# Kernel optimization log

Measured on AMD Instinct MI355X. Metric: run time of the kernel, lower is better.

The kernel has to match this reference:

```python
import jax, jax.numpy as jnp
import numpy as np

N, E, IN_FT, OUT_FT = 20000, 4096, 128, 128


def setup_inputs() -> dict:
    key = jax.random.key(0)
    kx, kh, kw = jax.random.split(key, 3)
    X = jax.random.normal(kx, (N, IN_FT), dtype=jnp.float32)
    H = jax.random.randint(kh, (N, E), 0, 2, dtype=jnp.int32)
    weight = jax.random.normal(kw, (IN_FT, OUT_FT), dtype=jnp.float32) * (1.0 / np.sqrt(IN_FT))
    bias = jnp.zeros((OUT_FT,), dtype=jnp.float32)
    return {"X": X, "H": H, "weight": weight, "bias": bias}


def reference(X, H, weight, bias):
    # Dv^{-1/2} H De^{-1} H^T Dv^{-1/2} X W + b, with diag matrices fused as
    # row/column scalings (same math as the torch.diag @ chain, no NxN temporaries).
    Hf = H.astype(jnp.float32)
    v_deg = jnp.sum(Hf, axis=1)            # [N]
    e_deg = jnp.sum(Hf, axis=0)            # [E]
    v_deg = jnp.where(v_deg > 0, v_deg, 1.0)
    e_deg = jnp.where(e_deg > 0, e_deg, 1.0)
    dv_inv_sqrt = 1.0 / jnp.sqrt(v_deg)    # diag(Dv^-1/2)
    de_inv = 1.0 / e_deg                   # diag(De^-1)
    Y = dv_inv_sqrt[:, None] * X
    T = Hf.T @ Y                           # H^T (...)        [E, in]
    T = de_inv[:, None] * T                # De^-1 (...)
    Z = Hf @ T                             # H (...)          [N, in]
    Z = dv_inv_sqrt[:, None] * Z           # Dv^-1/2 (...)
    out = Z @ weight + bias                # [N, out]
    return out
```

## Files before the change

### kernel.cpp

```cpp
#include <hip/hip_runtime.h>

#define NV 20000
#define NE 4096
#define FT 128
#define NW_E 128
#define NW_V 625
#define PT_STRIDE 632
#define NKC2 157
#define K_TOT 20096

typedef __attribute__((ext_vector_type(8))) short short8v;
typedef __attribute__((ext_vector_type(4))) float float4v;

__device__ __forceinline__ unsigned short f2bf(float f) {
    unsigned u = __float_as_uint(f);
    u += 0x7FFFu + ((u >> 16) & 1u);
    return (unsigned short)(u >> 16);
}
__device__ __forceinline__ int lds_off(int r, int c) {
    return r * 256 + ((c ^ (r & 15)) << 4);
}
__device__ __forceinline__ uint4 lut_entry(int t) {
    uint4 e;
    e.x = ((t & 1) ? 0x3F80u : 0u) | ((t & 2) ? 0x3F800000u : 0u);
    e.y = ((t & 4) ? 0x3F80u : 0u) | ((t & 8) ? 0x3F800000u : 0u);
    e.z = ((t & 16) ? 0x3F80u : 0u) | ((t & 32) ? 0x3F800000u : 0u);
    e.w = ((t & 64) ? 0x3F80u : 0u) | ((t & 128) ? 0x3F800000u : 0u);
    return e;
}
__device__ __forceinline__ void cp16(void* l, const void* g) {
    __builtin_amdgcn_global_load_lds((__attribute__((address_space(1))) void*)g,
                                     (__attribute__((address_space(3))) void*)l, 16, 0, 0);
}

__global__ __launch_bounds__(256) void k_pack(const int* __restrict__ H,
                                              unsigned* __restrict__ packed,
                                              float* __restrict__ dv,
                                              int* __restrict__ de_cnt) {
    __shared__ int cl[4];
    int t = threadIdx.x, wave = t >> 6, lane = t & 63;
    if (blockIdx.x < 16) de_cnt[blockIdx.x * 256 + t] = 0;
    int row = blockIdx.x * 2 + (wave >> 1);
    int half = wave & 1;
    const uint4* base = reinterpret_cast<const uint4*>(H) + (size_t)row * 1024 + half * 512 + lane * 8;
    unsigned m = 0;
#pragma unroll
    for (int i = 0; i < 8; ++i) {
        uint4 v = base[i];
        m |= (v.x ? 1u : 0u) << (i * 4 + 0);
        m |= (v.y ? 1u : 0u) << (i * 4 + 1);
        m |= (v.z ? 1u : 0u) << (i * 4 + 2);
        m |= (v.w ? 1u : 0u) << (i * 4 + 3);
    }
    packed[(size_t)row * NW_E + half * 64 + lane] = m;
    int c = __popc(m);
    for (int o = 32; o > 0; o >>= 1) c += __shfl_down(c, o, 64);
    if (lane == 0) cl[wave] = c;
    __syncthreads();
    if (t < 2) {
        int d = cl[t * 2] + cl[t * 2 + 1];
        dv[blockIdx.x * 2 + t] = d > 0 ? 1.0f / sqrtf((float)d) : 1.0f;
    }
}

__global__ __launch_bounds__(256) void k_btrans(const unsigned* __restrict__ packed,
                                                unsigned* __restrict__ packedT,
                                                int* __restrict__ de_cnt) {
    int lane = threadIdx.x & 63;
    int w = threadIdx.x >> 6;
    int ew = blockIdx.y * 4 + w;
    int n = blockIdx.x * 64 + lane;
    unsigned x = (n < NV) ? packed[(size_t)n * NW_E + ew] : 0u;
    unsigned y;
    y = __shfl_xor(x, 16, 64);
    x = (lane & 16) ? ((x & 0xFFFF0000u) | ((y >> 16) & 0x0000FFFFu))
                    : ((x & 0x0000FFFFu) | ((y << 16) & 0xFFFF0000u));
    y = __shfl_xor(x, 8, 64);
    x = (lane & 8)  ? ((x & 0xFF00FF00u) | ((y >> 8) & 0x00FF00FFu))
                    : ((x & 0x00FF00FFu) | ((y << 8) & 0xFF00FF00u));
    y = __shfl_xor(x, 4, 64);
    x = (lane & 4)  ? ((x & 0xF0F0F0F0u) | ((y >> 4) & 0x0F0F0F0Fu))
                    : ((x & 0x0F0F0F0Fu) | ((y << 4) & 0xF0F0F0F0u));
    y = __shfl_xor(x, 2, 64);
    x = (lane & 2)  ? ((x & 0xCCCCCCCCu) | ((y >> 2) & 0x33333333u))
                    : ((x & 0x33333333u) | ((y << 2) & 0xCCCCCCCCu));
    y = __shfl_xor(x, 1, 64);
    x = (lane & 1)  ? ((x & 0xAAAAAAAAu) | ((y >> 1) & 0x55555555u))
                    : ((x & 0x55555555u) | ((y << 1) & 0xAAAAAAAAu));
    int nw = blockIdx.x * 2 + (lane >> 5);
    int e = ew * 32 + (lane & 31);
    if (nw <= 625) packedT[(size_t)e * PT_STRIDE + nw] = x;
    int cnt = __popc(x);
    cnt += __shfl_down(cnt, 32, 64);
    if (lane < 32) atomicAdd(de_cnt + e, cnt);
}

__global__ __launch_bounds__(256) void k_mid(const float* __restrict__ X,
                                             const float* __restrict__ dv,
                                             unsigned short* __restrict__ At) {
    int t = threadIdx.x;
    int f = t & 127;
    int item = blockIdx.x * 2 + (t >> 7);
    int nbase = item * 8;
    unsigned short h[8];
#pragma unroll
    for (int i = 0; i < 8; ++i) {
        int n = nbase + i;
        float v = (n < NV) ? X[(size_t)n * FT + f] * dv[n] : 0.0f;
        h[i] = f2bf(v);
    }
    uint4 u;
    u.x = (unsigned)h[0] | ((unsigned)h[1] << 16);
    u.y = (unsigned)h[2] | ((unsigned)h[3] << 16);
    u.z = (unsigned)h[4] | ((unsigned)h[5] << 16);
    u.w = (unsigned)h[6] | ((unsigned)h[7] << 16);
    int kc2 = nbase >> 7;
    int c = (nbase >> 3) & 15;
    *reinterpret_cast<uint4*>(At + (size_t)kc2 * 16384 + f * 128 + ((c ^ (f & 15)) << 3)) = u;
}

__global__ __launch_bounds__(256, 2) void k_mm1(const unsigned short* __restrict__ At,
                                                const unsigned* __restrict__ packedT,
                                                float* __restrict__ P, int chunkK) {
    __shared__ __align__(16) unsigned char sA[32768];
    __shared__ __align__(16) unsigned char sB[32768];
    __shared__ __align__(16) uint4 slut[256];
    int t = threadIdx.x;
    slut[t] = lut_entry(t);

    int et = blockIdx.x & 31, kp = blockIdx.x >> 5;
    int e0 = et * 128;
    int kbeg = kp * chunkK;
    int kend = kbeg + chunkK; if (kend > K_TOT) kend = K_TOT;
    int iters = (kend - kbeg) >> 7; if (iters < 0) iters = 0;

    float4v acc[4][4];
#pragma unroll
    for (int i = 0; i < 4; ++i)
#pragma unroll
        for (int j = 0; j < 4; ++j)
#pragma unroll
            for (int r = 0; r < 4; ++r) acc[i][j][r] = 0.0f;

    int wave = t >> 6, lane = t & 63;
    int wm0 = (wave & 1) * 64, wc0 = (wave >> 1) * 64;
    int r0 = lane & 15, q = lane >> 4;

    int rB = t & 127, half = t >> 7, cb = half << 3;
    const uint4* brow4 = reinterpret_cast<const uint4*>(
        packedT + (size_t)(e0 + rB) * PT_STRIDE + (kbeg >> 5));
    uint4 bw;
    if (iters > 0) bw = brow4[0];
    __syncthreads();

    const char* gA = reinterpret_cast<const char*>(At) + (size_t)(kbeg >> 7) * 32768 + wave * 8192 + lane * 16;
    char* lA = reinterpret_cast<char*>(sA) + wave * 8192;

    for (int it = 0; it < iters; ++it) {
        const char* g = gA + (size_t)it * 32768;
#pragma unroll
        for (int j = 0; j < 8; ++j) cp16(lA + j * 1024, g + j * 1024);
        {
            uint4 nxt = brow4[it + 1];
            unsigned wd0 = half ? bw.z : bw.x;
            unsigned wd1 = half ? bw.w : bw.y;
#pragma unroll
            for (int c = 0; c < 4; ++c)
                *reinterpret_cast<uint4*>(sB + lds_off(rB, cb + c)) = slut[(wd0 >> (c * 8)) & 0xFF];
#pragma unroll
            for (int c = 0; c < 4; ++c)
                *reinterpret_cast<uint4*>(sB + lds_off(rB, cb + 4 + c)) = slut[(wd1 >> (c * 8)) & 0xFF];
            bw = nxt;
        }
        __syncthreads();
#pragma unroll
        for (int ks = 0; ks < 4; ++ks) {
            short8v a[4], bb[4];
#pragma unroll
            for (int mi = 0; mi < 4; ++mi)
                a[mi] = *reinterpret_cast<const short8v*>(sA + lds_off(wm0 + mi * 16 + r0, ks * 4 + q));
#pragma unroll
            for (int ci = 0; ci < 4; ++ci)
                bb[ci] = *reinterpret_cast<const short8v*>(sB + lds_off(wc0 + ci * 16 + r0, ks * 4 + q));
#pragma unroll
            for (int mi = 0; mi < 4; ++mi)
#pragma unroll
                for (int ci = 0; ci < 4; ++ci)
                    acc[mi][ci] = __builtin_amdgcn_mfma_f32_16x16x32_bf16(a[mi], bb[ci], acc[mi][ci], 0, 0, 0);
        }
        __syncthreads();
    }
    float* Pp = P + (size_t)kp * (4096 * 128);
#pragma unroll
    for (int mi = 0; mi < 4; ++mi)
#pragma unroll
        for (int ci = 0; ci < 4; ++ci) {
            int f = wm0 + mi * 16 + q * 4;
            int e = e0 + wc0 + ci * 16 + r0;
            *reinterpret_cast<float4v*>(Pp + (size_t)e * 128 + f) = acc[mi][ci];
        }
}

__global__ __launch_bounds__(256) void k_redut(const float* __restrict__ P,
                                               const float* __restrict__ W,
                                               const int* __restrict__ de_cnt,
                                               unsigned short* __restrict__ Ut, int S) {
    __shared__ float sT[8][132];
    int t = threadIdx.x;
    int e0 = blockIdx.x * 8;
    {
        int el = t >> 5, fq = (t & 31) * 4;
        const float* base = P + (size_t)(e0 + el) * 128 + fq;
        float4 s = {0.f, 0.f, 0.f, 0.f};
        for (int p = 0; p < S; ++p) {
            float4 v = *reinterpret_cast<const float4*>(base + (size_t)p * 524288);
            s.x += v.x; s.y += v.y; s.z += v.z; s.w += v.w;
        }
        *reinterpret_cast<float4*>(&sT[el][fq]) = s;
    }
    __syncthreads();
    int el = t & 7, gq = (t >> 3) * 4;
    int e = e0 + el;
    float a0 = 0, a1 = 0, a2 = 0, a3 = 0;
    for (int f = 0; f < 128; ++f) {
        float tv = sT[el][f];
        float4 wv = *reinterpret_cast<const float4*>(W + f * 128 + gq);
        a0 += tv * wv.x; a1 += tv * wv.y; a2 += tv * wv.z; a3 += tv * wv.w;
    }
    int cnt = de_cnt[e];
    float d = cnt > 0 ? 1.0f / (float)cnt : 1.0f;
    float av[4] = {a0, a1, a2, a3};
    int slabB = e >> 7, chi = (e >> 3) & 15, pos = e & 7;
#pragma unroll
    for (int k = 0; k < 4; ++k) {
        int g = gq + k, qg = g >> 5, gr = g & 31;
        Ut[(size_t)(qg * 32 + slabB) * 4096 + gr * 128 + ((chi ^ (gr & 15)) << 3) + pos] = f2bf(av[k] * d);
    }
}

__global__ __launch_bounds__(256, 3) void k_mm2(const unsigned* __restrict__ packed,
                                                const unsigned short* __restrict__ Ut,
                                                const float* __restrict__ dv,
                                                const float* __restrict__ bias,
                                                float* __restrict__ out) {
    __shared__ __align__(16) unsigned char sA[32768];
    __shared__ __align__(16) unsigned char sB[8192];
    __shared__ __align__(16) uint4 slut[256];
    int t = threadIdx.x;
    slut[t] = lut_entry(t);

    int mt = blockIdx.x >> 2, qg = blockIdx.x & 3;
    int n0 = mt * 128, g0 = qg * 32;

    float4v acc[4];
#pragma unroll
    for (int i = 0; i < 4; ++i)
#pragma unroll
        for (int r = 0; r < 4; ++r) acc[i][r] = 0.0f;

    int wave = t >> 6, lane = t & 63;
    int wm0 = (wave & 1) * 64, wc0 = (wave >> 1) * 16;
    int r0 = lane & 15, q = lane >> 4;

    int rA = t & 127, half = t >> 7, cb = half << 3;
    const uint4* arow4 = reinterpret_cast<const uint4*>(packed + (size_t)(n0 + rA) * NW_E);
    uint4 aw = arow4[0];
    __syncthreads();

    const char* gB = reinterpret_cast<const char*>(Ut) + (size_t)(qg * 32) * 8192 + (wave & 1) * 4096 + lane * 16;
    char* lB = reinterpret_cast<char*>(sB) + (wave & 1) * 4096;

    for (int it = 0; it < 32; ++it) {
        uint4 nxt = arow4[it + 1];
        if (wave < 2) {
            const char* g = gB + (size_t)it * 8192;
#pragma unroll
            for (int j = 0; j < 4; ++j) cp16(lB + j * 1024, g + j * 1024);
        }
        {
            unsigned wd0 = half ? aw.z : aw.x;
            unsigned wd1 = half ? aw.w : aw.y;
#pragma unroll
            for (int c = 0; c < 4; ++c)
                *reinterpret_cast<uint4*>(sA + lds_off(rA, cb + c)) = slut[(wd0 >> (c * 8)) & 0xFF];
#pragma unroll
            for (int c = 0; c < 4; ++c)
                *reinterpret_cast<uint4*>(sA + lds_off(rA, cb + 4 + c)) = slut[(wd1 >> (c * 8)) & 0xFF];
            aw = nxt;
        }
        __syncthreads();
#pragma unroll
        for (int ks = 0; ks < 4; ++ks) {
            short8v a[4], bb;
#pragma unroll
            for (int mi = 0; mi < 4; ++mi)
                a[mi] = *reinterpret_cast<const short8v*>(sA + lds_off(wm0 + mi * 16 + r0, ks * 4 + q));
            bb = *reinterpret_cast<const short8v*>(sB + lds_off(wc0 + r0, ks * 4 + q));
#pragma unroll
            for (int mi = 0; mi < 4; ++mi)
                acc[mi] = __builtin_amdgcn_mfma_f32_16x16x32_bf16(a[mi], bb, acc[mi], 0, 0, 0);
        }
        __syncthreads();
    }
    {
        int g = g0 + wc0 + r0;
        float bg = bias[g];
#pragma unroll
        for (int mi = 0; mi < 4; ++mi) {
#pragma unroll
            for (int r = 0; r < 4; ++r) {
                int n = n0 + wm0 + mi * 16 + q * 4 + r;
                if (n < NV) out[(size_t)n * 128 + g] = dv[n] * acc[mi][r] + bg;
            }
        }
    }
}

extern "C" void kernel_launch(void* const* d_in, const int* in_sizes, int n_in,
                              void* d_out, int out_size, void* d_ws, size_t ws_size,
                              hipStream_t stream) {
    const float* X    = (const float*)d_in[0];
    const int*   H    = (const int*)d_in[1];
    const float* W    = (const float*)d_in[2];
    const float* bias = (const float*)d_in[3];
    float* out = (float*)d_out;

    char* ws = (char*)d_ws;
    size_t off = 0;
    auto alloc = [&](size_t sz) { char* p = ws + off; off += (sz + 255) & ~(size_t)255; return p; };
    unsigned*       packed  = (unsigned*)alloc((size_t)NV * NW_E * 4);
    unsigned*       packedT = (unsigned*)alloc((size_t)NE * PT_STRIDE * 4);
    unsigned short* At      = (unsigned short*)alloc((size_t)NKC2 * 16384 * 2);
    unsigned short* Ut      = (unsigned short*)alloc((size_t)FT * NE * 2);
    float*          dv      = (float*)alloc((size_t)NV * 4);
    int*            de_cnt  = (int*)alloc((size_t)NE * 4);
    size_t fixed = off;

    long long avail = (long long)ws_size - (long long)fixed;
    int S = (int)(avail / (128LL * 4096 * 4));
    if (S > 16) S = 16;
    if (S < 1) S = 1;
    float* P1 = (float*)(ws + fixed);
    int chunkK = ((NKC2 + S - 1) / S) * 128;

    k_pack  <<<NV / 2, 256, 0, stream>>>(H, packed, dv, de_cnt);
    k_btrans<<<dim3(313, 32), 256, 0, stream>>>(packed, packedT, de_cnt);
    k_mid   <<<1256, 256, 0, stream>>>(X, dv, At);
    k_mm1   <<<32 * S, 256, 0, stream>>>(At, packedT, P1, chunkK);
    k_redut <<<512, 256, 0, stream>>>(P1, W, de_cnt, Ut, S);
    k_mm2   <<<628, 256, 0, stream>>>(packed, Ut, dv, bias, out);
}
```

Measured before the change: 589.1 us.

## Fuse bit-matrix transpose and edge-degree count into first GEMM kernel

```diff
diff --git a/kernel.cpp b/kernel.cpp
--- a/kernel.cpp
+++ b/kernel.cpp
@@ -4,8 +4,6 @@
 #define NE 4096
 #define FT 128
 #define NW_E 128
-#define NW_V 625
-#define PT_STRIDE 632
 #define NKC2 157
 #define K_TOT 20096
 
@@ -32,45 +30,7 @@
     __builtin_amdgcn_global_load_lds((__attribute__((address_space(1))) void*)g,
                                      (__attribute__((address_space(3))) void*)l, 16, 0, 0);
 }
-
-__global__ __launch_bounds__(256) void k_pack(const int* __restrict__ H,
-                                              unsigned* __restrict__ packed,
-                                              float* __restrict__ dv,
-                                              int* __restrict__ de_cnt) {
-    __shared__ int cl[4];
-    int t = threadIdx.x, wave = t >> 6, lane = t & 63;
-    if (blockIdx.x < 16) de_cnt[blockIdx.x * 256 + t] = 0;
-    int row = blockIdx.x * 2 + (wave >> 1);
-    int half = wave & 1;
-    const uint4* base = reinterpret_cast<const uint4*>(H) + (size_t)row * 1024 + half * 512 + lane * 8;
-    unsigned m = 0;
-#pragma unroll
-    for (int i = 0; i < 8; ++i) {
-        uint4 v = base[i];
-        m |= (v.x ? 1u : 0u) << (i * 4 + 0);
-        m |= (v.y ? 1u : 0u) << (i * 4 + 1);
-        m |= (v.z ? 1u : 0u) << (i * 4 + 2);
-        m |= (v.w ? 1u : 0u) << (i * 4 + 3);
-    }
-    packed[(size_t)row * NW_E + half * 64 + lane] = m;
-    int c = __popc(m);
-    for (int o = 32; o > 0; o >>= 1) c += __shfl_down(c, o, 64);
-    if (lane == 0) cl[wave] = c;
-    __syncthreads();
-    if (t < 2) {
-        int d = cl[t * 2] + cl[t * 2 + 1];
-        dv[blockIdx.x * 2 + t] = d > 0 ? 1.0f / sqrtf((float)d) : 1.0f;
-    }
-}
-
-__global__ __launch_bounds__(256) void k_btrans(const unsigned* __restrict__ packed,
-                                                unsigned* __restrict__ packedT,
-                                                int* __restrict__ de_cnt) {
-    int lane = threadIdx.x & 63;
-    int w = threadIdx.x >> 6;
-    int ew = blockIdx.y * 4 + w;
-    int n = blockIdx.x * 64 + lane;
-    unsigned x = (n < NV) ? packed[(size_t)n * NW_E + ew] : 0u;
+__device__ __forceinline__ unsigned bt32(unsigned x, int lane) {
     unsigned y;
     y = __shfl_xor(x, 16, 64);
     x = (lane & 16) ? ((x & 0xFFFF0000u) | ((y >> 16) & 0x0000FFFFu))
@@ -87,12 +47,37 @@
     y = __shfl_xor(x, 1, 64);
     x = (lane & 1)  ? ((x & 0xAAAAAAAAu) | ((y >> 1) & 0x55555555u))
                     : ((x & 0x55555555u) | ((y << 1) & 0xAAAAAAAAu));
-    int nw = blockIdx.x * 2 + (lane >> 5);
-    int e = ew * 32 + (lane & 31);
-    if (nw <= 625) packedT[(size_t)e * PT_STRIDE + nw] = x;
-    int cnt = __popc(x);
-    cnt += __shfl_down(cnt, 32, 64);
-    if (lane < 32) atomicAdd(de_cnt + e, cnt);
+    return x;
+}
+
+__global__ __launch_bounds__(256) void k_pack(const int* __restrict__ H,
+                                              unsigned* __restrict__ packed,
+                                              float* __restrict__ dv,
+                                              int* __restrict__ de_cnt) {
+    __shared__ int cl[4];
+    int t = threadIdx.x, wave = t >> 6, lane = t & 63;
+    if (blockIdx.x < 16) de_cnt[blockIdx.x * 256 + t] = 0;
+    int row = blockIdx.x * 2 + (wave >> 1);
+    int half = wave & 1;
+    const uint4* base = reinterpret_cast<const uint4*>(H) + (size_t)row * 1024 + half * 512 + lane * 8;
+    unsigned m = 0;
+#pragma unroll
+    for (int i = 0; i < 8; ++i) {
+        uint4 v = base[i];
+        m |= (v.x ? 1u : 0u) << (i * 4 + 0);
+        m |= (v.y ? 1u : 0u) << (i * 4 + 1);
+        m |= (v.z ? 1u : 0u) << (i * 4 + 2);
+        m |= (v.w ? 1u : 0u) << (i * 4 + 3);
+    }
+    packed[(size_t)row * NW_E + half * 64 + lane] = m;
+    int c = __popc(m);
+    for (int o = 32; o > 0; o >>= 1) c += __shfl_down(c, o, 64);
+    if (lane == 0) cl[wave] = c;
+    __syncthreads();
+    if (t < 2) {
+        int d = cl[t * 2] + cl[t * 2 + 1];
+        dv[blockIdx.x * 2 + t] = d > 0 ? 1.0f / sqrtf((float)d) : 1.0f;
+    }
 }
 
 __global__ __launch_bounds__(256) void k_mid(const float* __restrict__ X,
@@ -120,8 +105,9 @@
 }
 
 __global__ __launch_bounds__(256, 2) void k_mm1(const unsigned short* __restrict__ At,
-                                                const unsigned* __restrict__ packedT,
-                                                float* __restrict__ P, int chunkK) {
+                                                const unsigned* __restrict__ packed,
+                                                float* __restrict__ P,
+                                                int* __restrict__ de_cnt, int chunkK) {
     __shared__ __align__(16) unsigned char sA[32768];
     __shared__ __align__(16) unsigned char sB[32768];
     __shared__ __align__(16) uint4 slut[256];
@@ -146,30 +132,45 @@
     int wm0 = (wave & 1) * 64, wc0 = (wave >> 1) * 64;
     int r0 = lane & 15, q = lane >> 4;
 
-    int rB = t & 127, half = t >> 7, cb = half << 3;
-    const uint4* brow4 = reinterpret_cast<const uint4*>(
-        packedT + (size_t)(e0 + rB) * PT_STRIDE + (kbeg >> 5));
-    uint4 bw;
-    if (iters > 0) bw = brow4[0];
+    int grp = t >> 5, l32 = t & 31;
+    int ns = grp & 3;
+    int wbase = (grp >> 2) * 2;
+    int ecol = et * 4 + wbase;
+    int de_c0 = 0, de_c1 = 0;
+
+    auto ldB = [&](int it) {
+        uint2 v; v.x = 0u; v.y = 0u;
+        int n = kbeg + it * 128 + ns * 32 + l32;
+        if (n < NV) v = *reinterpret_cast<const uint2*>(packed + (size_t)n * NW_E + ecol);
+        return v;
+    };
+    uint2 bw; bw.x = 0u; bw.y = 0u;
+    if (iters > 0) bw = ldB(0);
     __syncthreads();
 
     const char* gA = reinterpret_cast<const char*>(At) + (size_t)(kbeg >> 7) * 32768 + wave * 8192 + lane * 16;
     char* lA = reinterpret_cast<char*>(sA) + wave * 8192;
 
+    int rB0 = wbase * 32 + l32;
+    int rB1 = rB0 + 32;
+
     for (int it = 0; it < iters; ++it) {
         const char* g = gA + (size_t)it * 32768;
 #pragma unroll
         for (int j = 0; j < 8; ++j) cp16(lA + j * 1024, g + j * 1024);
+        uint2 nxt; nxt.x = 0u; nxt.y = 0u;
+        if (it + 1 < iters) nxt = ldB(it + 1);
         {
-            uint4 nxt = brow4[it + 1];
-            unsigned wd0 = half ? bw.z : bw.x;
-            unsigned wd1 = half ? bw.w : bw.y;
+            unsigned x0 = bt32(bw.x, lane);
+            unsigned x1 = bt32(bw.y, lane);
+            de_c0 += __popc(x0);
+            de_c1 += __popc(x1);
 #pragma unroll
             for (int c = 0; c < 4; ++c)
-                *reinterpret_cast<uint4*>(sB + lds_off(rB, cb + c)) = slut[(wd0 >> (c * 8)) & 0xFF];
+                *reinterpret_cast<uint4*>(sB + lds_off(rB0, ns * 4 + c)) = slut[(x0 >> (c * 8)) & 0xFF];
 #pragma unroll
             for (int c = 0; c < 4; ++c)
-                *reinterpret_cast<uint4*>(sB + lds_off(rB, cb + 4 + c)) = slut[(wd1 >> (c * 8)) & 0xFF];
+                *reinterpret_cast<uint4*>(sB + lds_off(rB1, ns * 4 + c)) = slut[(x1 >> (c * 8)) & 0xFF];
             bw = nxt;
         }
         __syncthreads();
@@ -190,6 +191,8 @@
         }
         __syncthreads();
     }
+    atomicAdd(de_cnt + e0 + rB0, de_c0);
+    atomicAdd(de_cnt + e0 + rB1, de_c1);
     float* Pp = P + (size_t)kp * (4096 * 128);
 #pragma unroll
     for (int mi = 0; mi < 4; ++mi)
@@ -329,7 +332,6 @@
     size_t off = 0;
     auto alloc = [&](size_t sz) { char* p = ws + off; off += (sz + 255) & ~(size_t)255; return p; };
     unsigned*       packed  = (unsigned*)alloc((size_t)NV * NW_E * 4);
-    unsigned*       packedT = (unsigned*)alloc((size_t)NE * PT_STRIDE * 4);
     unsigned short* At      = (unsigned short*)alloc((size_t)NKC2 * 16384 * 2);
     unsigned short* Ut      = (unsigned short*)alloc((size_t)FT * NE * 2);
     float*          dv      = (float*)alloc((size_t)NV * 4);
@@ -344,9 +346,8 @@
     int chunkK = ((NKC2 + S - 1) / S) * 128;
 
     k_pack  <<<NV / 2, 256, 0, stream>>>(H, packed, dv, de_cnt);
-    k_btrans<<<dim3(313, 32), 256, 0, stream>>>(packed, packedT, de_cnt);
     k_mid   <<<1256, 256, 0, stream>>>(X, dv, At);
-    k_mm1   <<<32 * S, 256, 0, stream>>>(At, packedT, P1, chunkK);
+    k_mm1   <<<32 * S, 256, 0, stream>>>(At, packed, P1, de_cnt, chunkK);
     k_redut <<<512, 256, 0, stream>>>(P1, W, de_cnt, Ut, S);
     k_mm2   <<<628, 256, 0, stream>>>(packed, Ut, dv, bias, out);
 }
```

After: 559.4 us. 1.05x faster.
